# Kernel optimization log

Hardware: AMD Instinct MI355X
Metric: run time of the kernel (lower is better)

Reference implementation:

```python
import jax, jax.numpy as jnp
import numpy as np

B, N, E, G, V = 8, 512, 8192, 1024, 100000
HD, FIN, BN_EPS = 1024, 20, 1e-5


def setup_inputs() -> dict:
    key = jax.random.key(0)
    ks = jax.random.split(key, 8)
    return {
        'h': jax.random.normal(ks[0], (B, N, FIN), jnp.float32),
        'src': jax.random.randint(ks[1], (B, E), 0, N, jnp.int32),
        'dst': jax.random.randint(ks[2], (B, E), 0, N, jnp.int32),
        'gPos': jax.random.randint(ks[3], (B, G), 0, V, jnp.int32),
        'allDBGEmb': jax.random.normal(ks[4], (V, HD), jnp.float32),
        'fc_init_w': jax.random.normal(ks[5], (HD, FIN), jnp.float32) * (1.0 / np.sqrt(FIN)),
        'fc_init_b': jnp.zeros((HD,), jnp.float32),
        'bn1_g': jnp.ones((HD,), jnp.float32),
        'bn1_b': jnp.zeros((HD,), jnp.float32),
        'bn2_g': jnp.ones((HD,), jnp.float32),
        'bn2_b': jnp.zeros((HD,), jnp.float32),
        'fc_w': jax.random.normal(ks[6], (128, 2 * HD), jnp.float32) * (1.0 / np.sqrt(2 * HD)),
        'fc_b': jnp.zeros((128,), jnp.float32),
        'bn3_g': jnp.ones((128,), jnp.float32),
        'bn3_b': jnp.zeros((128,), jnp.float32),
        'fc2_w': jax.random.normal(ks[7], (1, 128), jnp.float32) * (1.0 / np.sqrt(128)),
        'fc2_b': jnp.zeros((1,), jnp.float32),
    }


def _bn(x, g, b):
    # BatchNorm1d in training mode: batch statistics over axis 0 (biased var)
    mu = x.mean(0)
    var = ((x - mu) ** 2).mean(0)
    return (x - mu) * jax.lax.rsqrt(var + BN_EPS) * g + b


def _gin_mean(x, s, d):
    # GINConv(None, 'mean') with eps=0: h_v + mean_{u in N(v)} h_u
    sums = jax.ops.segment_sum(x[s], d, num_segments=N)  # [N, HD]
    deg = jax.ops.segment_sum(jnp.ones((E, 1), x.dtype), d, num_segments=N)
    return x + jnp.where(deg > 0, sums / jnp.maximum(deg, 1.0), 0.0)


def reference(h, src, dst, gPos, allDBGEmb, fc_init_w, fc_init_b,
              bn1_g, bn1_b, bn2_g, bn2_b, fc_w, fc_b, bn3_g, bn3_b,
              fc2_w, fc2_b):
    def per_graph(hq, s, d, gp):
        x = hq @ fc_init_w.T + fc_init_b                      # [N, HD]
        x = jax.nn.relu(_bn(_gin_mean(x, s, d), bn1_g, bn1_b))
        x = jax.nn.relu(_bn(_gin_mean(x, s, d), bn2_g, bn2_b))
        qemb = x.mean(0)                                      # dgl.mean_nodes
        gEmb = allDBGEmb[gp]                                  # [G, HD]
        H = jnp.concatenate([jnp.broadcast_to(qemb, (G, HD)), gEmb], axis=1)
        h2 = jax.nn.relu(_bn(H @ fc_w.T + fc_b, bn3_g, bn3_b))
        return jax.nn.sigmoid(h2 @ fc2_w.T + fc2_b).reshape(-1)  # [G]

    return jax.vmap(per_graph)(h, src, dst, gPos)  # [B, G]
```

## Files before the change

kernel.cpp:

```cpp
#include <hip/hip_runtime.h>
#include <hip/hip_bf16.h>

#define B_ 8
#define G_ 1024
#define HD_ 1024
#define EPS_ 1e-5f


typedef __attribute__((ext_vector_type(8))) short bf16x8;
typedef __attribute__((ext_vector_type(4))) float f32x4;

__device__ inline short bf1(float x) {
    return (short)__builtin_bit_cast(unsigned short, __float2bfloat16(x));
}
__device__ inline bf16x8 cvt8(float4 a, float4 b) {
    bf16x8 o;
    o[0] = bf1(a.x); o[1] = bf1(a.y); o[2] = bf1(a.z); o[3] = bf1(a.w);
    o[4] = bf1(b.x); o[5] = bf1(b.y); o[6] = bf1(b.z); o[7] = bf1(b.w);
    return o;
}
__device__ inline float bf2f(unsigned short u) {
    return __builtin_bit_cast(float, (unsigned)u << 16);
}

__global__ __launch_bounds__(256) void k_w2cvt(const float* __restrict__ fc_w,
                                               short* __restrict__ w2arr) {
    int gid = blockIdx.x * 256 + threadIdx.x;
    int kt = gid >> 9;
    int jblk = (gid >> 6) & 7;
    int lane = gid & 63;
    int j = jblk * 16 + (lane & 15);
    int k = kt * 32 + (lane >> 4) * 8;
    const float4* sp = (const float4*)&fc_w[(size_t)j * (2 * HD_) + HD_ + k];
    *(bf16x8*)&w2arr[(size_t)gid * 8] = cvt8(sp[0], sp[1]);
}

#define SLABW 258

__global__ __launch_bounds__(512) void k_gemm(const int* __restrict__ gPos,
                                              const float* __restrict__ emb,
                                              const short* __restrict__ w2arr,
                                              short* __restrict__ zb,
                                              float* __restrict__ ps,
                                              float* __restrict__ pq) {
    int b = blockIdx.y, gblk = blockIdx.x;
    int gbase = gblk * 32;
    int tid = threadIdx.x;
    int jq = tid >> 6, lane = tid & 63;
    int l15 = lane & 15, kb = lane >> 4;

    __shared__ short As[128 * SLABW];

    {
        int arow = tid >> 4, acp = tid & 15;
        const float* abase = emb + (size_t)gPos[b * G_ + gbase + arow] * HD_;
#pragma unroll
        for (int i = 0; i < 8; ++i) {
            int k = i * 128 + acp * 8;
            const float4* ap = (const float4*)(abase + k);
            *(bf16x8*)&As[(i * 16 + acp) * SLABW + arow * 8] = cvt8(ap[0], ap[1]);
        }
    }
    __syncthreads();

    f32x4 acc0 = {0.f, 0.f, 0.f, 0.f}, acc1 = {0.f, 0.f, 0.f, 0.f};
#pragma unroll 4
    for (int kt = 0; kt < 32; ++kt) {
        int f = kt * 8 + jq;
        bf16x8 bv = *(const bf16x8*)&w2arr[((size_t)f * 64 + lane) * 8];
        bf16x8 a0 = *(const bf16x8*)&As[(kt * 4 + kb) * SLABW + l15 * 8];
        bf16x8 a1 = *(const bf16x8*)&As[(kt * 4 + kb) * SLABW + (16 + l15) * 8];
        acc0 = __builtin_amdgcn_mfma_f32_16x16x32_bf16(a0, bv, acc0, 0, 0, 0);
        acc1 = __builtin_amdgcn_mfma_f32_16x16x32_bf16(a1, bv, acc1, 0, 0, 0);
    }

    int jcol = jq * 16 + l15;
    float s = 0.f, q = 0.f;
#pragma unroll
    for (int r = 0; r < 4; ++r) {
        float v0 = acc0[r], v1 = acc1[r];
        int g0 = gbase + kb * 4 + r;
        int g1 = g0 + 16;
        zb[(size_t)(b * G_ + g0) * 128 + jcol] = bf1(v0);
        zb[(size_t)(b * G_ + g1) * 128 + jcol] = bf1(v1);
        s += v0 + v1;
        q += v0 * v0 + v1 * v1;
    }
    s += __shfl_xor(s, 16, 64); s += __shfl_xor(s, 32, 64);
    q += __shfl_xor(q, 16, 64); q += __shfl_xor(q, 32, 64);
    if (lane < 16) {
        ps[(b * 32 + gblk) * 128 + jcol] = s;
        pq[(b * 32 + gblk) * 128 + jcol] = q;
    }
}

__global__ __launch_bounds__(256) void k_final(const short* __restrict__ zb,
                                               const float* __restrict__ ps,
                                               const float* __restrict__ pq,
                                               const float* __restrict__ g3,
                                               const float* __restrict__ b3,
                                               const float* __restrict__ fc2w,
                                               const float* __restrict__ fc2b,
                                               float* __restrict__ out) {
    int b = blockIdx.y, gseg = blockIdx.x;
    int tid = threadIdx.x, wave = tid >> 6, lane = tid & 63;
    __shared__ float scL[128], shL[128];
    if (tid < 128) {
        int j = tid;
        float s = 0.f, q = 0.f;
#pragma unroll 8
        for (int t = 0; t < 32; ++t) {
            s += ps[(b * 32 + t) * 128 + j];
            q += pq[(b * 32 + t) * 128 + j];
        }
        float mu = s * (1.f / G_);
        float var = q * (1.f / G_) - mu * mu;
        float sc = g3[j] * rsqrtf(var + EPS_);
        scL[j] = sc;
        shL[j] = b3[j] - mu * sc;
    }
    __syncthreads();
    int j0 = lane * 2;
    float sc0 = scL[j0], sc1 = scL[j0 + 1];
    float sh0 = shL[j0], sh1 = shL[j0 + 1];
    float w0 = fc2w[j0], w1 = fc2w[j0 + 1], bias = fc2b[0];
#pragma unroll
    for (int it = 0; it < 16; ++it) {
        int g = gseg * 64 + it * 4 + wave;
        const ushort2* zr = (const ushort2*)(zb + (size_t)(b * G_ + g) * 128);
        ushort2 u = zr[lane];
        float acc = fmaxf(fmaf(bf2f(u.x), sc0, sh0), 0.f) * w0 +
                    fmaxf(fmaf(bf2f(u.y), sc1, sh1), 0.f) * w1;
        acc += __shfl_xor(acc, 32, 64);
        acc += __shfl_xor(acc, 16, 64);
        acc += __shfl_xor(acc, 8, 64);
        acc += __shfl_xor(acc, 4, 64);
        acc += __shfl_xor(acc, 2, 64);
        acc += __shfl_xor(acc, 1, 64);
        if (lane == 0) out[b * G_ + g] = 1.f / (1.f + expf(-(acc + bias)));
    }
}

extern "C" void kernel_launch(void* const* d_in, const int* in_sizes, int n_in,
                              void* d_out, int out_size, void* d_ws, size_t ws_size,
                              hipStream_t stream) {
    const int*   gPos = (const int*)d_in[3];
    const float* emb  = (const float*)d_in[4];
    const float* fc_w = (const float*)d_in[11];
    const float* bn3g = (const float*)d_in[13];
    const float* bn3b = (const float*)d_in[14];
    const float* fc2w = (const float*)d_in[15];
    const float* fc2b = (const float*)d_in[16];
    float* out = (float*)d_out;

    char* w = (char*)d_ws;
    short* zb    = (short*)w; w += (size_t)B_ * G_ * 128 * 2;
    short* w2arr = (short*)w; w += (size_t)128 * HD_ * 2;
    float* ps    = (float*)w; w += (size_t)B_ * 32 * 128 * 4;
    float* pq    = (float*)w; w += (size_t)B_ * 32 * 128 * 4;

    k_w2cvt<<<64, 256, 0, stream>>>(fc_w, w2arr);
    k_gemm<<<dim3(32, B_), 512, 0, stream>>>(gPos, emb, w2arr, zb, ps, pq);
    k_final<<<dim3(16, B_), 256, 0, stream>>>(zb, ps, pq, bn3g, bn3b, fc2w, fc2b, out);
}
```

Before: 31.07 us.

## Double-buffer gathered embedding slabs in LDS and store GEMM output as fp32

The GEMM kernel no longer stages the whole 32x1024 gathered embedding tile in LDS before computing. It now streams the K dimension in eight 128-wide chunks through two small LDS buffers, loading and converting the next chunk while MFMAs run on the current one. Gather indices are staged in shared memory first. This shrinks the LDS footprint, which may raise occupancy and overlap gather latency with compute, at the cost of a barrier per chunk. Separately, the intermediate z is now written and read as fp32 instead of bf16. That removes a rounding step but doubles that buffer's memory traffic.

```diff
diff --git a/kernel.cpp b/kernel.cpp
--- a/kernel.cpp
+++ b/kernel.cpp
@@ -19,9 +19,6 @@
     o[4] = bf1(b.x); o[5] = bf1(b.y); o[6] = bf1(b.z); o[7] = bf1(b.w);
     return o;
 }
-__device__ inline float bf2f(unsigned short u) {
-    return __builtin_bit_cast(float, (unsigned)u << 16);
-}
 
 __global__ __launch_bounds__(256) void k_w2cvt(const float* __restrict__ fc_w,
                                                short* __restrict__ w2arr) {
@@ -35,12 +32,12 @@
     *(bf16x8*)&w2arr[(size_t)gid * 8] = cvt8(sp[0], sp[1]);
 }
 
-#define SLABW 258
+#define ASLAB 258
 
 __global__ __launch_bounds__(512) void k_gemm(const int* __restrict__ gPos,
                                               const float* __restrict__ emb,
                                               const short* __restrict__ w2arr,
-                                              short* __restrict__ zb,
+                                              float* __restrict__ z,
                                               float* __restrict__ ps,
                                               float* __restrict__ pq) {
     int b = blockIdx.y, gblk = blockIdx.x;
@@ -49,29 +46,39 @@
     int jq = tid >> 6, lane = tid & 63;
     int l15 = lane & 15, kb = lane >> 4;
 
-    __shared__ short As[128 * SLABW];
+    __shared__ int gidx[32];
+    __shared__ short As[2][16 * ASLAB];
+
+    if (tid < 32) gidx[tid] = gPos[b * G_ + gbase + tid];
+    __syncthreads();
+
+    int arow = tid >> 4, acp = tid & 15;
+    const float* abase = emb + (size_t)gidx[arow] * HD_;
+
+    f32x4 acc0 = {0.f, 0.f, 0.f, 0.f}, acc1 = {0.f, 0.f, 0.f, 0.f};
 
     {
-        int arow = tid >> 4, acp = tid & 15;
-        const float* abase = emb + (size_t)gPos[b * G_ + gbase + arow] * HD_;
-#pragma unroll
-        for (int i = 0; i < 8; ++i) {
-            int k = i * 128 + acp * 8;
-            const float4* ap = (const float4*)(abase + k);
-            *(bf16x8*)&As[(i * 16 + acp) * SLABW + arow * 8] = cvt8(ap[0], ap[1]);
-        }
+        const float4* ap = (const float4*)(abase + acp * 8);
+        *(bf16x8*)&As[0][acp * ASLAB + arow * 8] = cvt8(ap[0], ap[1]);
     }
     __syncthreads();
 
-    f32x4 acc0 = {0.f, 0.f, 0.f, 0.f}, acc1 = {0.f, 0.f, 0.f, 0.f};
-#pragma unroll 4
-    for (int kt = 0; kt < 32; ++kt) {
-        int f = kt * 8 + jq;
-        bf16x8 bv = *(const bf16x8*)&w2arr[((size_t)f * 64 + lane) * 8];
-        bf16x8 a0 = *(const bf16x8*)&As[(kt * 4 + kb) * SLABW + l15 * 8];
-        bf16x8 a1 = *(const bf16x8*)&As[(kt * 4 + kb) * SLABW + (16 + l15) * 8];
-        acc0 = __builtin_amdgcn_mfma_f32_16x16x32_bf16(a0, bv, acc0, 0, 0, 0);
-        acc1 = __builtin_amdgcn_mfma_f32_16x16x32_bf16(a1, bv, acc1, 0, 0, 0);
+    for (int p = 0; p < 8; ++p) {
+        int cur = p & 1;
+        if (p < 7) {
+            const float4* ap = (const float4*)(abase + (p + 1) * 128 + acp * 8);
+            *(bf16x8*)&As[cur ^ 1][acp * ASLAB + arow * 8] = cvt8(ap[0], ap[1]);
+        }
+#pragma unroll
+        for (int kt = 0; kt < 4; ++kt) {
+            int f = (p * 4 + kt) * 8 + jq;
+            bf16x8 bv = *(const bf16x8*)&w2arr[((size_t)f * 64 + lane) * 8];
+            bf16x8 a0 = *(const bf16x8*)&As[cur][(kt * 4 + kb) * ASLAB + l15 * 8];
+            bf16x8 a1 = *(const bf16x8*)&As[cur][(kt * 4 + kb) * ASLAB + (16 + l15) * 8];
+            acc0 = __builtin_amdgcn_mfma_f32_16x16x32_bf16(a0, bv, acc0, 0, 0, 0);
+            acc1 = __builtin_amdgcn_mfma_f32_16x16x32_bf16(a1, bv, acc1, 0, 0, 0);
+        }
+        __syncthreads();
     }
 
     int jcol = jq * 16 + l15;
@@ -81,8 +88,8 @@
         float v0 = acc0[r], v1 = acc1[r];
         int g0 = gbase + kb * 4 + r;
         int g1 = g0 + 16;
-        zb[(size_t)(b * G_ + g0) * 128 + jcol] = bf1(v0);
-        zb[(size_t)(b * G_ + g1) * 128 + jcol] = bf1(v1);
+        z[(size_t)(b * G_ + g0) * 128 + jcol] = v0;
+        z[(size_t)(b * G_ + g1) * 128 + jcol] = v1;
         s += v0 + v1;
         q += v0 * v0 + v1 * v1;
     }
@@ -94,7 +101,7 @@
     }
 }
 
-__global__ __launch_bounds__(256) void k_final(const short* __restrict__ zb,
+__global__ __launch_bounds__(256) void k_final(const float* __restrict__ z,
                                                const float* __restrict__ ps,
                                                const float* __restrict__ pq,
                                                const float* __restrict__ g3,
@@ -127,10 +134,10 @@
 #pragma unroll
     for (int it = 0; it < 16; ++it) {
         int g = gseg * 64 + it * 4 + wave;
-        const ushort2* zr = (const ushort2*)(zb + (size_t)(b * G_ + g) * 128);
-        ushort2 u = zr[lane];
-        float acc = fmaxf(fmaf(bf2f(u.x), sc0, sh0), 0.f) * w0 +
-                    fmaxf(fmaf(bf2f(u.y), sc1, sh1), 0.f) * w1;
+        const float2* zr = (const float2*)(z + (size_t)(b * G_ + g) * 128);
+        float2 u = zr[lane];
+        float acc = fmaxf(fmaf(u.x, sc0, sh0), 0.f) * w0 +
+                    fmaxf(fmaf(u.y, sc1, sh1), 0.f) * w1;
         acc += __shfl_xor(acc, 32, 64);
         acc += __shfl_xor(acc, 16, 64);
         acc += __shfl_xor(acc, 8, 64);
@@ -154,12 +161,12 @@
     float* out = (float*)d_out;
 
     char* w = (char*)d_ws;
-    short* zb    = (short*)w; w += (size_t)B_ * G_ * 128 * 2;
+    float* z     = (float*)w; w += (size_t)B_ * G_ * 128 * 4;
     short* w2arr = (short*)w; w += (size_t)128 * HD_ * 2;
     float* ps    = (float*)w; w += (size_t)B_ * 32 * 128 * 4;
     float* pq    = (float*)w; w += (size_t)B_ * 32 * 128 * 4;
 
     k_w2cvt<<<64, 256, 0, stream>>>(fc_w, w2arr);
-    k_gemm<<<dim3(32, B_), 512, 0, stream>>>(gPos, emb, w2arr, zb, ps, pq);
-    k_final<<<dim3(16, B_), 256, 0, stream>>>(zb, ps, pq, bn3g, bn3b, fc2w, fc2b, out);
+    k_gemm<<<dim3(32, B_), 512, 0, stream>>>(gPos, emb, w2arr, z, ps, pq);
+    k_final<<<dim3(16, B_), 256, 0, stream>>>(z, ps, pq, bn3g, bn3b, fc2w, fc2b, out);
 }
```

Result: slower. 35.54 us (+14.4%).
